# Optimization experiments

Measured on AMD Instinct MI355X. Metric: run time of the kernel, lower is better.

Reference implementation:

```python
import jax, jax.numpy as jnp
import numpy as np

Z_DIM = 128
E_L_STEPS = 60
E_L_STEP_SIZE = 0.4
E_ALPHA = 1.0
E_BETA = 1.0
E_GAMMA = 1.0
E_PRIOR_SIG = 1.0
E_L_WITH_NOISE = True
BATCH = 65536


def _linear_init(k, fin, fout):
    # torch nn.Linear default: U(-1/sqrt(fin), 1/sqrt(fin)) for weight and bias
    s = 1.0 / np.sqrt(fin)
    kw, kb = jax.random.split(k)
    W = jax.random.uniform(kw, (fin, fout), minval=-s, maxval=s, dtype=jnp.float32)
    b = jax.random.uniform(kb, (fout,), minval=-s, maxval=s, dtype=jnp.float32)
    return W, b


def setup_inputs() -> dict:
    key = jax.random.key(0)
    k1, k2, k3, kz = jax.random.split(key, 4)
    W1, b1 = _linear_init(k1, Z_DIM, 512)
    W2, b2 = _linear_init(k2, 512, 64)
    W3, b3 = _linear_init(k3, 64, 1)
    z = jax.random.normal(kz, (BATCH, Z_DIM), dtype=jnp.float32)
    return {"z": z, "W1": W1, "b1": b1, "W2": W2, "b2": b2, "W3": W3, "b3": b3}


def _energy_sum(z, W1, b1, W2, b2, W3, b3):
    # NetE: Linear(z_dim,512) -> GELU -> Linear(512,64) -> GELU -> Linear(64,1)
    h = jax.nn.gelu(z @ W1 + b1, approximate=False)
    h = jax.nn.gelu(h @ W2 + b2, approximate=False)
    return jnp.sum(h @ W3 + b3)


def reference(z, W1, b1, W2, b2, W3, b3):
    noise_key = jax.random.key(42)
    coef_grad = -E_ALPHA * 0.5 * E_L_STEP_SIZE * E_L_STEP_SIZE
    coef_prior = -E_BETA * 0.5 * E_L_STEP_SIZE * E_L_STEP_SIZE / (E_PRIOR_SIG * E_PRIOR_SIG)
    grad_fn = jax.grad(lambda zz: _energy_sum(zz, W1, b1, W2, b2, W3, b3))

    def step(zz, i):
        g = grad_fn(zz)  # dE/dz, shape [B, z_dim]
        upd = coef_grad * g + coef_prior * zz
        if E_L_WITH_NOISE:
            noise = jax.random.normal(jax.random.fold_in(noise_key, i), zz.shape, zz.dtype)
            upd = upd + E_GAMMA * E_L_STEP_SIZE * noise
        return zz + upd, None

    z_final, _ = jax.lax.scan(step, z, jnp.arange(E_L_STEPS))
    return z_final
```

## Files before the change

kernel.cpp:

```cpp
#include <hip/hip_runtime.h>
#include <stdint.h>


#define BATCH   65536
#define ZDIM    128
#define H1      512
#define H2      64
#define NSTEP   60
#define COEF    (-0.08f)

using bf16x8 = __attribute__((ext_vector_type(8))) short;
using f32x4  = __attribute__((ext_vector_type(4))) float;

#define MFMA16(a, b, c) __builtin_amdgcn_mfma_f32_16x16x32_bf16((a), (b), (c), 0, 0, 0)

__device__ __forceinline__ uint32_t rotl32(uint32_t v, int s) {
  return (v << s) | (v >> (32 - s));
}

__device__ __forceinline__ void tf2x32(uint32_t k0, uint32_t k1,
                                       uint32_t x0, uint32_t x1,
                                       uint32_t& o0, uint32_t& o1) {
  const uint32_t k2 = k0 ^ k1 ^ 0x1BD11BDAu;
  x0 += k0; x1 += k1;
  x0 += x1; x1 = rotl32(x1, 13); x1 ^= x0;
  x0 += x1; x1 = rotl32(x1, 15); x1 ^= x0;
  x0 += x1; x1 = rotl32(x1, 26); x1 ^= x0;
  x0 += x1; x1 = rotl32(x1,  6); x1 ^= x0;
  x0 += k1; x1 += k2 + 1u;
  x0 += x1; x1 = rotl32(x1, 17); x1 ^= x0;
  x0 += x1; x1 = rotl32(x1, 29); x1 ^= x0;
  x0 += x1; x1 = rotl32(x1, 16); x1 ^= x0;
  x0 += x1; x1 = rotl32(x1, 24); x1 ^= x0;
  x0 += k2; x1 += k0 + 2u;
  x0 += x1; x1 = rotl32(x1, 13); x1 ^= x0;
  x0 += x1; x1 = rotl32(x1, 15); x1 ^= x0;
  x0 += x1; x1 = rotl32(x1, 26); x1 ^= x0;
  x0 += x1; x1 = rotl32(x1,  6); x1 ^= x0;
  x0 += k0; x1 += k1 + 3u;
  x0 += x1; x1 = rotl32(x1, 17); x1 ^= x0;
  x0 += x1; x1 = rotl32(x1, 29); x1 ^= x0;
  x0 += x1; x1 = rotl32(x1, 16); x1 ^= x0;
  x0 += x1; x1 = rotl32(x1, 24); x1 ^= x0;
  x0 += k1; x1 += k2 + 4u;
  x0 += x1; x1 = rotl32(x1, 13); x1 ^= x0;
  x0 += x1; x1 = rotl32(x1, 15); x1 ^= x0;
  x0 += x1; x1 = rotl32(x1, 26); x1 ^= x0;
  x0 += x1; x1 = rotl32(x1,  6); x1 ^= x0;
  x0 += k2; x1 += k0 + 5u;
  o0 = x0; o1 = x1;
}

__device__ __forceinline__ float normal_from_bits(uint32_t bits) {
  float u01 = __uint_as_float((bits >> 9) | 0x3F800000u) - 1.0f;
  const float lo = -0.99999994f;
  float u = fmaxf(lo, u01 * 2.0f + lo);
  float w = -__logf(fmaf(-u, u, 1.0f));
  float p;
  if (w < 5.0f) {
    w -= 2.5f;
    p =             2.81022636e-08f;
    p = fmaf(p, w,  3.43273939e-07f);
    p = fmaf(p, w, -3.5233877e-06f);
    p = fmaf(p, w, -4.39150654e-06f);
    p = fmaf(p, w,  0.00021858087f);
    p = fmaf(p, w, -0.00125372503f);
    p = fmaf(p, w, -0.00417768164f);
    p = fmaf(p, w,  0.246640727f);
    p = fmaf(p, w,  1.50140941f);
  } else {
    w = sqrtf(w) - 3.0f;
    p =            -0.000200214257f;
    p = fmaf(p, w,  0.000100950558f);
    p = fmaf(p, w,  0.00134934322f);
    p = fmaf(p, w, -0.00367342844f);
    p = fmaf(p, w,  0.00573950773f);
    p = fmaf(p, w, -0.0076224613f);
    p = fmaf(p, w,  0.00943887047f);
    p = fmaf(p, w,  1.00167406f);
    p = fmaf(p, w,  2.83297682f);
  }
  return 1.41421356f * (p * u);
}

struct N4 { float v[4]; };
__device__ __forceinline__ N4 noise4(uint32_t k0, uint32_t k1, uint32_t f0) {
  const uint32_t k2 = k0 ^ k1 ^ 0x1BD11BDAu;
  uint32_t x0[4], x1[4];
  #pragma unroll
  for (int i = 0; i < 4; ++i) { x0[i] = k0; x1[i] = (f0 + 128u * (uint32_t)i) + k1; }
#define TFG(ra, rb, rc, rd, ia, ib, ic)                                        \
  _Pragma("unroll")                                                            \
  for (int i = 0; i < 4; ++i) {                                                \
    x0[i] += x1[i]; x1[i] = rotl32(x1[i], ra); x1[i] ^= x0[i];                 \
    x0[i] += x1[i]; x1[i] = rotl32(x1[i], rb); x1[i] ^= x0[i];                 \
    x0[i] += x1[i]; x1[i] = rotl32(x1[i], rc); x1[i] ^= x0[i];                 \
    x0[i] += x1[i]; x1[i] = rotl32(x1[i], rd); x1[i] ^= x0[i];                 \
    x0[i] += (ia); x1[i] += (ib) + (ic); }
  TFG(13, 15, 26,  6, k1, k2, 1u)
  TFG(17, 29, 16, 24, k2, k0, 2u)
  TFG(13, 15, 26,  6, k0, k1, 3u)
  TFG(17, 29, 16, 24, k1, k2, 4u)
  TFG(13, 15, 26,  6, k2, k0, 5u)
#undef TFG
  N4 r;
  #pragma unroll
  for (int i = 0; i < 4; ++i) r.v[i] = normal_from_bits(x0[i] ^ x1[i]);
  return r;
}

__device__ __forceinline__ float sigm(float y) {
  return __fdividef(1.0f, 1.0f + __expf(-y));
}
__device__ __forceinline__ float gelu_fast(float x) { return x * sigm(1.702f * x); }
__device__ __forceinline__ float gelu_grad_fast(float x) {
  float s = sigm(1.702f * x);
  return fmaf(1.702f * x, s * (1.0f - s), s);
}

__device__ __forceinline__ float gelu_exact(float x) {
  return 0.5f * x * (1.0f + erff(x * 0.70710678f));
}
__device__ __forceinline__ float gelu_grad_exact(float x) {
  float u   = x * 0.70710678f;
  float cdf = 0.5f * (1.0f + erff(u));
  float pdf = 0.39894228040143267f * expf(-u * u);
  return fmaf(x, pdf, cdf);
}

__device__ __forceinline__ unsigned short f2bf(float x) {
  return (unsigned short)(__float_as_uint(x) >> 16);
}

__global__ void pack_b(const float* __restrict__ src, unsigned short* __restrict__ dst,
                       int K, int N, int trans, int total, float scale) {
  int o = blockIdx.x * 256 + threadIdx.x;
  if (o >= total) return;
  int t   = o >> 9;
  int rem = o & 511;
  int l = rem >> 3, j = rem & 7;
  int nb = N >> 4;
  int kb = t / nb, cb = t - kb * nb;
  int k = kb * 32 + (l >> 4) * 8 + j;
  int n = cb * 16 + (l & 15);
  float v = trans ? src[(size_t)n * K + k] : src[(size_t)k * N + n];
  dst[o] = f2bf(scale * v);
}

__device__ __forceinline__ bf16x8 lds_frag(const unsigned short* lds, int row,
                                           int ebase, int rowElems) {
  int e = ebase ^ ((row & 7) << 3);
  return *(const bf16x8*)(lds + row * rowElems + e);
}
__device__ __forceinline__ bf16x8 load_frag(const unsigned short* p, int tile, int lane) {
  return *(const bf16x8*)(p + tile * 512 + lane * 8);
}

__global__ __launch_bounds__(256, 4) void langevin_mfma(
    const float* __restrict__ z0,
    const float* __restrict__ b1,
    const float* __restrict__ b2,
    const float* __restrict__ W3,
    const unsigned short* __restrict__ W1p,
    const unsigned short* __restrict__ W2p,
    const unsigned short* __restrict__ W2Tp,
    const unsigned short* __restrict__ W1Tp,
    float* __restrict__ out)
{
  __shared__ unsigned short Zlds[64 * 128];
  __shared__ unsigned short HEu[64 * 64];
  __shared__ unsigned short D2lds[64 * 64];
  __shared__ float b1lds[512];
  __shared__ float b2lds[64];
  __shared__ float w3lds[64];

  const int tid  = threadIdx.x;
  const int lane = tid & 63;
  const int wid  = tid >> 6;
  const int wg   = blockIdx.x;

  b1lds[tid] = b1[tid];
  b1lds[tid + 256] = b1[tid + 256];
  if (tid < 64) { b2lds[tid] = b2[tid]; w3lds[tid] = W3[tid]; }
  __syncthreads();

  const int rbase = wid * 16 + ((lane >> 4) << 2);
  const int clane = lane & 15;
  const int arow  = wid * 16 + clane;
  const int ahi   = (lane >> 4) << 3;

  f32x4 zacc[8];
  #pragma unroll
  for (int t = 0; t < 8; ++t) {
    #pragma unroll
    for (int i = 0; i < 4; ++i) {
      int row = rbase + i;
      int col = t * 16 + clane;
      float zv = z0[(size_t)(wg * 64 + row) * ZDIM + col];
      zacc[t][i] = zv;
      Zlds[row * 128 + (col ^ ((row & 7) << 3))] = f2bf(zv);
    }
  }

  for (int step = 0; step < NSTEP; ++step) {
    uint32_t fk0, fk1;
    tf2x32(0u, 42u, 0u, (uint32_t)step, fk0, fk1);

    f32x4 a2acc[4];
    #pragma unroll
    for (int ct = 0; ct < 4; ++ct) {
      float bb = b2lds[ct * 16 + clane];
      a2acc[ct] = f32x4{bb, bb, bb, bb};
    }

    #pragma unroll 1
    for (int jb = 0; jb < 8; ++jb) {
      __syncthreads();
      #pragma unroll
      for (int ct = 0; ct < 4; ++ct) {
        f32x4 acc = f32x4{0.f, 0.f, 0.f, 0.f};
        #pragma unroll
        for (int kb = 0; kb < 4; ++kb) {
          bf16x8 za = lds_frag(Zlds, arow, kb * 32 + ahi, 128);
          acc = MFMA16(za, load_frag(W1p, kb * 32 + jb * 4 + ct, lane), acc);
        }
        float bb = b1lds[jb * 64 + ct * 16 + clane];
        #pragma unroll
        for (int i = 0; i < 4; ++i) {
          int row = rbase + i;
          int c   = ct * 16 + clane;
          HEu[row * 64 + (c ^ ((row & 7) << 3))] = f2bf(gelu_fast(acc[i] + bb));
        }
      }
      #pragma unroll
      for (int kb = 0; kb < 2; ++kb) {
        bf16x8 ha = lds_frag(HEu, arow, kb * 32 + ahi, 64);
        #pragma unroll
        for (int ct = 0; ct < 4; ++ct)
          a2acc[ct] = MFMA16(ha, load_frag(W2p, (jb * 2 + kb) * 4 + ct, lane), a2acc[ct]);
      }
    }

    #pragma unroll
    for (int ct = 0; ct < 4; ++ct) {
      float w3v = w3lds[ct * 16 + clane];
      #pragma unroll
      for (int i = 0; i < 4; ++i) {
        int row = rbase + i;
        int c   = ct * 16 + clane;
        D2lds[row * 64 + (c ^ ((row & 7) << 3))] = f2bf(w3v * gelu_grad_fast(a2acc[ct][i]));
      }
    }

    {
      const uint32_t gs0 = (uint32_t)(wg * 64 + rbase) * 128u;
      #pragma unroll
      for (int t = 0; t < 8; ++t) {
        N4 nz = noise4(fk0, fk1, gs0 + (uint32_t)(t * 16 + clane));
        #pragma unroll
        for (int i = 0; i < 4; ++i) {
          float zv = zacc[t][i];
          zacc[t][i] = fmaf(0.4f, nz.v[i], fmaf(COEF, zv, zv));
        }
      }
    }

    #pragma unroll 1
    for (int jb = 0; jb < 8; ++jb) {
      __syncthreads();
      bf16x8 d2a0 = lds_frag(D2lds, arow, 0  + ahi, 64);
      bf16x8 d2a1 = lds_frag(D2lds, arow, 32 + ahi, 64);
      #pragma unroll
      for (int ct = 0; ct < 4; ++ct) {
        f32x4 eacc = f32x4{0.f, 0.f, 0.f, 0.f};
        eacc = MFMA16(d2a0, load_frag(W2Tp,      jb * 4 + ct, lane), eacc);
        eacc = MFMA16(d2a1, load_frag(W2Tp, 32 + jb * 4 + ct, lane), eacc);
        f32x4 a1acc = f32x4{0.f, 0.f, 0.f, 0.f};
        #pragma unroll
        for (int kb = 0; kb < 4; ++kb) {
          bf16x8 za = lds_frag(Zlds, arow, kb * 32 + ahi, 128);
          a1acc = MFMA16(za, load_frag(W1p, kb * 32 + jb * 4 + ct, lane), a1acc);
        }
        float bb = b1lds[jb * 64 + ct * 16 + clane];
        #pragma unroll
        for (int i = 0; i < 4; ++i) {
          int row = rbase + i;
          int c   = ct * 16 + clane;
          float ev = eacc[i] * gelu_grad_fast(a1acc[i] + bb);
          HEu[row * 64 + (c ^ ((row & 7) << 3))] = f2bf(ev);
        }
      }
      #pragma unroll
      for (int kb = 0; kb < 2; ++kb) {
        bf16x8 ea = lds_frag(HEu, arow, kb * 32 + ahi, 64);
        #pragma unroll
        for (int t = 0; t < 8; ++t)
          zacc[t] = MFMA16(ea, load_frag(W1Tp, (jb * 2 + kb) * 8 + t, lane), zacc[t]);
      }
    }

    #pragma unroll
    for (int t = 0; t < 8; ++t) {
      #pragma unroll
      for (int i = 0; i < 4; ++i) {
        int row = rbase + i;
        int col = t * 16 + clane;
        Zlds[row * 128 + (col ^ ((row & 7) << 3))] = f2bf(zacc[t][i]);
      }
    }
  }

  #pragma unroll
  for (int t = 0; t < 8; ++t) {
    #pragma unroll
    for (int i = 0; i < 4; ++i) {
      int row = rbase + i;
      out[(size_t)(wg * 64 + row) * ZDIM + t * 16 + clane] = zacc[t][i];
    }
  }
}

__global__ void transpose_w1(const float* __restrict__ W1, float* __restrict__ W1T) {
  int o = blockIdx.x * 256 + threadIdx.x;
  int j = o >> 7, k = o & 127;
  W1T[o] = W1[k * H1 + j];
}

__device__ __forceinline__ float normal_from_bits_exact(uint32_t bits) {
  float u01 = __uint_as_float((bits >> 9) | 0x3F800000u) - 1.0f;
  const float lo = -0.99999994f;
  float u = fmaxf(lo, u01 * 2.0f + lo);
  float w = -log1pf(-u * u);
  float p;
  if (w < 5.0f) {
    w -= 2.5f;
    p =             2.81022636e-08f;
    p = fmaf(p, w,  3.43273939e-07f);
    p = fmaf(p, w, -3.5233877e-06f);
    p = fmaf(p, w, -4.39150654e-06f);
    p = fmaf(p, w,  0.00021858087f);
    p = fmaf(p, w, -0.00125372503f);
    p = fmaf(p, w, -0.00417768164f);
    p = fmaf(p, w,  0.246640727f);
    p = fmaf(p, w,  1.50140941f);
  } else {
    w = sqrtf(w) - 3.0f;
    p =            -0.000200214257f;
    p = fmaf(p, w,  0.000100950558f);
    p = fmaf(p, w,  0.00134934322f);
    p = fmaf(p, w, -0.00367342844f);
    p = fmaf(p, w,  0.00573950773f);
    p = fmaf(p, w, -0.0076224613f);
    p = fmaf(p, w,  0.00943887047f);
    p = fmaf(p, w,  1.00167406f);
    p = fmaf(p, w,  2.83297682f);
  }
  return 1.41421356f * (p * u);
}

__global__ __launch_bounds__(256, 1) void langevin_scalar(
    const float* __restrict__ z0, const float* __restrict__ b1,
    const float* __restrict__ W2, const float* __restrict__ b2,
    const float* __restrict__ W3, const float* __restrict__ W1T,
    float* __restrict__ out)
{
  __shared__ float nbuf[256 * 33];
  const int tid = threadIdx.x;
  const uint32_t b = (uint32_t)blockIdx.x * 256u + (uint32_t)tid;
  float z[ZDIM];
  #pragma unroll
  for (int k = 0; k < ZDIM; ++k) z[k] = z0[(size_t)b * ZDIM + k];
  for (int step = 0; step < NSTEP; ++step) {
    uint32_t fk0, fk1;
    tf2x32(0u, 42u, 0u, (uint32_t)step, fk0, fk1);
    float acc2[H2];
    #pragma unroll
    for (int c = 0; c < H2; ++c) acc2[c] = b2[c];
    #pragma unroll 2
    for (int j = 0; j < H1; ++j) {
      const float* __restrict__ w = W1T + j * ZDIM;
      float s0 = 0.f, s1 = 0.f, s2 = 0.f, s3 = 0.f;
      #pragma unroll
      for (int k = 0; k < ZDIM; k += 4) {
        s0 = fmaf(z[k + 0], w[k + 0], s0); s1 = fmaf(z[k + 1], w[k + 1], s1);
        s2 = fmaf(z[k + 2], w[k + 2], s2); s3 = fmaf(z[k + 3], w[k + 3], s3);
      }
      float a1 = b1[j] + ((s0 + s1) + (s2 + s3));
      float h  = gelu_exact(a1);
      const float* __restrict__ w2r = W2 + j * H2;
      #pragma unroll
      for (int c = 0; c < H2; ++c) acc2[c] = fmaf(h, w2r[c], acc2[c]);
    }
    #pragma unroll
    for (int c = 0; c < H2; ++c) acc2[c] = W3[c] * gelu_grad_exact(acc2[c]);
    float g[ZDIM];
    #pragma unroll
    for (int k = 0; k < ZDIM; ++k) g[k] = 0.f;
    for (int j = 0; j < H1; ++j) {
      const float* __restrict__ w = W1T + j * ZDIM;
      float s0 = 0.f, s1 = 0.f, s2 = 0.f, s3 = 0.f;
      #pragma unroll
      for (int k = 0; k < ZDIM; k += 4) {
        s0 = fmaf(z[k + 0], w[k + 0], s0); s1 = fmaf(z[k + 1], w[k + 1], s1);
        s2 = fmaf(z[k + 2], w[k + 2], s2); s3 = fmaf(z[k + 3], w[k + 3], s3);
      }
      float a1 = b1[j] + ((s0 + s1) + (s2 + s3));
      const float* __restrict__ w2r = W2 + j * H2;
      float d0 = 0.f, d1 = 0.f, d2 = 0.f, d3 = 0.f;
      #pragma unroll
      for (int c = 0; c < H2; c += 4) {
        d0 = fmaf(acc2[c + 0], w2r[c + 0], d0); d1 = fmaf(acc2[c + 1], w2r[c + 1], d1);
        d2 = fmaf(acc2[c + 2], w2r[c + 2], d2); d3 = fmaf(acc2[c + 3], w2r[c + 3], d3);
      }
      float eps = ((d0 + d1) + (d2 + d3)) * gelu_grad_exact(a1);
      #pragma unroll
      for (int k = 0; k < ZDIM; ++k) g[k] = fmaf(eps, w[k], g[k]);
    }
    const uint32_t base = b * (uint32_t)ZDIM;
    #pragma unroll
    for (int kc = 0; kc < 4; ++kc) {
      for (int kk = 0; kk < 32; ++kk) {
        uint32_t f = base + (uint32_t)(kc * 32 + kk);
        uint32_t r0, r1;
        tf2x32(fk0, fk1, 0u, f, r0, r1);
        nbuf[tid * 33 + kk] = normal_from_bits_exact(r0 ^ r1);
      }
      #pragma unroll
      for (int i = 0; i < 32; ++i) {
        const int k = kc * 32 + i;
        z[k] += COEF * g[k] + COEF * z[k] + 0.4f * nbuf[tid * 33 + i];
      }
    }
  }
  #pragma unroll
  for (int k = 0; k < ZDIM; ++k) out[(size_t)b * ZDIM + k] = z[k];
}

extern "C" void kernel_launch(void* const* d_in, const int* in_sizes, int n_in,
                              void* d_out, int out_size, void* d_ws, size_t ws_size,
                              hipStream_t stream) {
  (void)in_sizes; (void)n_in; (void)out_size;

  const float* z0 = (const float*)d_in[0];
  const float* W1 = (const float*)d_in[1];
  const float* b1 = (const float*)d_in[2];
  const float* W2 = (const float*)d_in[3];
  const float* b2 = (const float*)d_in[4];
  const float* W3 = (const float*)d_in[5];
  float* out = (float*)d_out;

  const size_t NEED = 196608u * 2u;
  if (ws_size >= NEED) {
    unsigned short* W1p  = (unsigned short*)d_ws;
    unsigned short* W2p  = W1p  + 65536;
    unsigned short* W2Tp = W2p  + 32768;
    unsigned short* W1Tp = W2Tp + 32768;

    hipLaunchKernelGGL(pack_b, dim3(256), dim3(256), 0, stream, W1, W1p,  128, 512, 0, 65536, 1.0f);
    hipLaunchKernelGGL(pack_b, dim3(128), dim3(256), 0, stream, W2, W2p,  512,  64, 0, 32768, 1.0f);
    hipLaunchKernelGGL(pack_b, dim3(128), dim3(256), 0, stream, W2, W2Tp,  64, 512, 1, 32768, 1.0f);
    hipLaunchKernelGGL(pack_b, dim3(256), dim3(256), 0, stream, W1, W1Tp, 512, 128, 1, 65536, COEF);
    hipLaunchKernelGGL(langevin_mfma, dim3(BATCH / 64), dim3(256), 0, stream,
                       z0, b1, b2, W3, W1p, W2p, W2Tp, W1Tp, out);
  } else {
    float* W1T = (float*)d_ws;
    hipLaunchKernelGGL(transpose_w1, dim3(256), dim3(256), 0, stream, W1, W1T);
    hipLaunchKernelGGL(langevin_scalar, dim3(BATCH / 256), dim3(256), 0, stream,
                       z0, b1, W2, b2, W3, W1T, out);
  }
}
```

Before: 6.470 ms.

## Split each 64-row tile across wave pairs with 512-thread blocks

Doubles the block to 512 threads and gives each pair of waves the same 16 rows, with each wave owning half of the output columns in every GEMM stage. Per-wave z and hidden accumulators shrink by half, which cuts register pressure and may raise the number of resident waves and latency hiding. Because the hidden tiles in LDS are now written by two waves, extra block-wide barriers are added inside both inner loops. Scheduling barriers are also placed in the noise loop. The trade-off is more synchronisation and duplicated A-fragment LDS reads across the wave pairs.

```diff
diff --git a/kernel.cpp b/kernel.cpp
--- a/kernel.cpp
+++ b/kernel.cpp
@@ -156,7 +156,7 @@
   return *(const bf16x8*)(p + tile * 512 + lane * 8);
 }
 
-__global__ __launch_bounds__(256, 4) void langevin_mfma(
+__global__ __launch_bounds__(512, 4) void langevin_mfma(
     const float* __restrict__ z0,
     const float* __restrict__ b1,
     const float* __restrict__ b2,
@@ -177,27 +177,28 @@
   const int tid  = threadIdx.x;
   const int lane = tid & 63;
   const int wid  = tid >> 6;
+  const int rg   = wid >> 1;
+  const int ch   = wid & 1;
   const int wg   = blockIdx.x;
 
   b1lds[tid] = b1[tid];
-  b1lds[tid + 256] = b1[tid + 256];
   if (tid < 64) { b2lds[tid] = b2[tid]; w3lds[tid] = W3[tid]; }
-  __syncthreads();
-
-  const int rbase = wid * 16 + ((lane >> 4) << 2);
+
+  const int rbase = rg * 16 + ((lane >> 4) << 2);
   const int clane = lane & 15;
-  const int arow  = wid * 16 + clane;
+  const int arow  = rg * 16 + clane;
   const int ahi   = (lane >> 4) << 3;
 
-  f32x4 zacc[8];
-  #pragma unroll
-  for (int t = 0; t < 8; ++t) {
+  f32x4 zacc[4];
+  #pragma unroll
+  for (int tl = 0; tl < 4; ++tl) {
+    const int t = ch * 4 + tl;
     #pragma unroll
     for (int i = 0; i < 4; ++i) {
       int row = rbase + i;
       int col = t * 16 + clane;
       float zv = z0[(size_t)(wg * 64 + row) * ZDIM + col];
-      zacc[t][i] = zv;
+      zacc[tl][i] = zv;
       Zlds[row * 128 + (col ^ ((row & 7) << 3))] = f2bf(zv);
     }
   }
@@ -206,18 +207,19 @@
     uint32_t fk0, fk1;
     tf2x32(0u, 42u, 0u, (uint32_t)step, fk0, fk1);
 
-    f32x4 a2acc[4];
-    #pragma unroll
-    for (int ct = 0; ct < 4; ++ct) {
-      float bb = b2lds[ct * 16 + clane];
-      a2acc[ct] = f32x4{bb, bb, bb, bb};
+    f32x4 a2acc[2];
+    #pragma unroll
+    for (int ctl = 0; ctl < 2; ++ctl) {
+      float bb = b2lds[(ch * 2 + ctl) * 16 + clane];
+      a2acc[ctl] = f32x4{bb, bb, bb, bb};
     }
 
     #pragma unroll 1
     for (int jb = 0; jb < 8; ++jb) {
       __syncthreads();
       #pragma unroll
-      for (int ct = 0; ct < 4; ++ct) {
+      for (int ctl = 0; ctl < 2; ++ctl) {
+        const int ct = ch * 2 + ctl;
         f32x4 acc = f32x4{0.f, 0.f, 0.f, 0.f};
         #pragma unroll
         for (int kb = 0; kb < 4; ++kb) {
@@ -232,36 +234,40 @@
           HEu[row * 64 + (c ^ ((row & 7) << 3))] = f2bf(gelu_fast(acc[i] + bb));
         }
       }
+      __syncthreads();
       #pragma unroll
       for (int kb = 0; kb < 2; ++kb) {
         bf16x8 ha = lds_frag(HEu, arow, kb * 32 + ahi, 64);
         #pragma unroll
-        for (int ct = 0; ct < 4; ++ct)
-          a2acc[ct] = MFMA16(ha, load_frag(W2p, (jb * 2 + kb) * 4 + ct, lane), a2acc[ct]);
-      }
-    }
-
-    #pragma unroll
-    for (int ct = 0; ct < 4; ++ct) {
+        for (int ctl = 0; ctl < 2; ++ctl)
+          a2acc[ctl] = MFMA16(ha, load_frag(W2p, (jb * 2 + kb) * 4 + ch * 2 + ctl, lane),
+                              a2acc[ctl]);
+      }
+    }
+
+    #pragma unroll
+    for (int ctl = 0; ctl < 2; ++ctl) {
+      const int ct = ch * 2 + ctl;
       float w3v = w3lds[ct * 16 + clane];
       #pragma unroll
       for (int i = 0; i < 4; ++i) {
         int row = rbase + i;
         int c   = ct * 16 + clane;
-        D2lds[row * 64 + (c ^ ((row & 7) << 3))] = f2bf(w3v * gelu_grad_fast(a2acc[ct][i]));
+        D2lds[row * 64 + (c ^ ((row & 7) << 3))] = f2bf(w3v * gelu_grad_fast(a2acc[ctl][i]));
       }
     }
 
     {
       const uint32_t gs0 = (uint32_t)(wg * 64 + rbase) * 128u;
       #pragma unroll
-      for (int t = 0; t < 8; ++t) {
-        N4 nz = noise4(fk0, fk1, gs0 + (uint32_t)(t * 16 + clane));
+      for (int tl = 0; tl < 4; ++tl) {
+        N4 nz = noise4(fk0, fk1, gs0 + (uint32_t)((ch * 4 + tl) * 16 + clane));
         #pragma unroll
         for (int i = 0; i < 4; ++i) {
-          float zv = zacc[t][i];
-          zacc[t][i] = fmaf(0.4f, nz.v[i], fmaf(COEF, zv, zv));
+          float zv = zacc[tl][i];
+          zacc[tl][i] = fmaf(0.4f, nz.v[i], fmaf(COEF, zv, zv));
         }
+        __builtin_amdgcn_sched_barrier(0);
       }
     }
 
@@ -271,7 +277,8 @@
       bf16x8 d2a0 = lds_frag(D2lds, arow, 0  + ahi, 64);
       bf16x8 d2a1 = lds_frag(D2lds, arow, 32 + ahi, 64);
       #pragma unroll
-      for (int ct = 0; ct < 4; ++ct) {
+      for (int ctl = 0; ctl < 2; ++ctl) {
+        const int ct = ch * 2 + ctl;
         f32x4 eacc = f32x4{0.f, 0.f, 0.f, 0.f};
         eacc = MFMA16(d2a0, load_frag(W2Tp,      jb * 4 + ct, lane), eacc);
         eacc = MFMA16(d2a1, load_frag(W2Tp, 32 + jb * 4 + ct, lane), eacc);
@@ -290,32 +297,36 @@
           HEu[row * 64 + (c ^ ((row & 7) << 3))] = f2bf(ev);
         }
       }
+      __syncthreads();
       #pragma unroll
       for (int kb = 0; kb < 2; ++kb) {
         bf16x8 ea = lds_frag(HEu, arow, kb * 32 + ahi, 64);
         #pragma unroll
-        for (int t = 0; t < 8; ++t)
-          zacc[t] = MFMA16(ea, load_frag(W1Tp, (jb * 2 + kb) * 8 + t, lane), zacc[t]);
-      }
-    }
-
-    #pragma unroll
-    for (int t = 0; t < 8; ++t) {
+        for (int tl = 0; tl < 4; ++tl)
+          zacc[tl] = MFMA16(ea, load_frag(W1Tp, (jb * 2 + kb) * 8 + ch * 4 + tl, lane),
+                            zacc[tl]);
+      }
+    }
+
+    #pragma unroll
+    for (int tl = 0; tl < 4; ++tl) {
+      const int t = ch * 4 + tl;
       #pragma unroll
       for (int i = 0; i < 4; ++i) {
         int row = rbase + i;
         int col = t * 16 + clane;
-        Zlds[row * 128 + (col ^ ((row & 7) << 3))] = f2bf(zacc[t][i]);
-      }
-    }
-  }
-
-  #pragma unroll
-  for (int t = 0; t < 8; ++t) {
+        Zlds[row * 128 + (col ^ ((row & 7) << 3))] = f2bf(zacc[tl][i]);
+      }
+    }
+  }
+
+  #pragma unroll
+  for (int tl = 0; tl < 4; ++tl) {
+    const int t = ch * 4 + tl;
     #pragma unroll
     for (int i = 0; i < 4; ++i) {
       int row = rbase + i;
-      out[(size_t)(wg * 64 + row) * ZDIM + t * 16 + clane] = zacc[t][i];
+      out[(size_t)(wg * 64 + row) * ZDIM + t * 16 + clane] = zacc[tl][i];
     }
   }
 }
@@ -460,7 +471,7 @@
     hipLaunchKernelGGL(pack_b, dim3(128), dim3(256), 0, stream, W2, W2p,  512,  64, 0, 32768, 1.0f);
     hipLaunchKernelGGL(pack_b, dim3(128), dim3(256), 0, stream, W2, W2Tp,  64, 512, 1, 32768, 1.0f);
     hipLaunchKernelGGL(pack_b, dim3(256), dim3(256), 0, stream, W1, W1Tp, 512, 128, 1, 65536, COEF);
-    hipLaunchKernelGGL(langevin_mfma, dim3(BATCH / 64), dim3(256), 0, stream,
+    hipLaunchKernelGGL(langevin_mfma, dim3(BATCH / 64), dim3(512), 0, stream,
                        z0, b1, b2, W3, W1p, W2p, W2Tp, W1Tp, out);
   } else {
     float* W1T = (float*)d_ws;
```

After: 5.784 ms (median of 3 runs). -10.6%, faster.
